# Kernel optimization log

Measured on AMD Instinct MI355X. Metric: run time of the kernel, lower is better.

## Reference

```python
import math
import jax, jax.numpy as jnp
import numpy as np

B, T, C, NH = 2, 2048, 2048, 16
HD = C // NH  # 128


def _quantize_int6(key, out_f, in_f):
    """Replicates Int6LinearDynamic.reset_parameters/_quantize_update."""
    w = jax.random.normal(key, (out_f, in_f), jnp.float32) * (1.0 / math.sqrt(in_f))
    max_val = jnp.clip(jnp.max(jnp.abs(w), axis=1, keepdims=True), 1e-5)
    scale = max_val / 31.0
    w_int = jnp.clip(jnp.round(w / scale), -32, 31).astype(jnp.int8)
    return w_int, scale.squeeze(1)  # [out,in] int8, [out] f32


def setup_inputs() -> dict:
    key = jax.random.key(0)
    k_x, k_a, k_p = jax.random.split(key, 3)
    attn_w, attn_scales = _quantize_int6(k_a, 3 * C, C)
    proj_w, proj_scales = _quantize_int6(k_p, C, C)
    return {
        "x": jax.random.normal(k_x, (B, T, C), jnp.float32),
        "attn_w": attn_w,
        "attn_scales": attn_scales,
        "proj_w": proj_w,
        "proj_scales": proj_scales,
        "qk_gain": jnp.float32(1.0),
    }


def _l2norm(t):
    # F.normalize(p=2, dim=-1, eps=1e-12)
    n = jnp.sqrt(jnp.sum(t * t, axis=-1, keepdims=True))
    return t / jnp.maximum(n, 1e-12)


def reference(x, attn_w, attn_scales, proj_w, proj_scales, qk_gain):
    # dequantized int6 GEMM: w = int8 * per-row scale
    wa = attn_w.astype(jnp.float32) * attn_scales[:, None]  # [3C, C]
    qkv = jnp.einsum("btc,oc->bto", x, wa)                   # [B,T,3C]
    q, k, v = jnp.split(qkv, 3, axis=2)

    def heads(t):  # [B,T,C] -> [B,NH,T,HD]
        return t.reshape(B, T, NH, HD).transpose(0, 2, 1, 3)

    q, k, v = heads(q), heads(k), heads(v)
    q = _l2norm(q) * qk_gain
    k = _l2norm(k) * qk_gain

    # causal SDPA, default scale 1/sqrt(head_dim)
    scores = jnp.einsum("bhqd,bhkd->bhqk", q, k) / math.sqrt(HD)
    causal = jnp.tril(jnp.ones((T, T), dtype=bool))
    scores = jnp.where(causal, scores, -jnp.inf)
    attn = jax.nn.softmax(scores, axis=-1)
    y = jnp.einsum("bhqk,bhkd->bhqd", attn, v)               # [B,NH,T,HD]
    y = y.transpose(0, 2, 1, 3).reshape(B, T, C)

    wp = proj_w.astype(jnp.float32) * proj_scales[:, None]   # [C, C]
    return jnp.einsum("btc,oc->bto", y, wp)
```

## Files before the change

### kernel.cpp

```cpp
#include <hip/hip_runtime.h>


#define DEVINL __device__ __forceinline__

typedef unsigned short u16;
typedef __bf16 bf16x8 __attribute__((ext_vector_type(8)));
typedef float  f32x4  __attribute__((ext_vector_type(4)));
typedef float  f32x16 __attribute__((ext_vector_type(16)));
typedef short  short8 __attribute__((ext_vector_type(8)));
typedef u16    u16x4  __attribute__((ext_vector_type(4)));
typedef unsigned uint4x __attribute__((ext_vector_type(4)));

static constexpr int T_  = 2048;
static constexpr int C_  = 2048;
static constexpr int TC3 = 6144;

DEVINL u16 f2bf(float f) {
  union { float f; unsigned u; } v; v.f = f;
  unsigned r = v.u + 0x7FFFu + ((v.u >> 16) & 1u);
  return (u16)(r >> 16);
}
DEVINL float bf2f(u16 s) {
  union { unsigned u; float f; } v; v.u = ((unsigned)s) << 16;
  return v.f;
}
DEVINL bf16x8 ld8(const u16* p) {
  return __builtin_bit_cast(bf16x8, *(const short8*)p);
}
DEVINL f32x4 mfma16(bf16x8 a, bf16x8 b, f32x4 c) {
  return __builtin_amdgcn_mfma_f32_16x16x32_bf16(a, b, c, 0, 0, 0);
}
DEVINL f32x16 mfma32(bf16x8 a, bf16x8 b, f32x16 c) {
  return __builtin_amdgcn_mfma_f32_32x32x16_bf16(a, b, c, 0, 0, 0);
}
DEVINL void async_cp16(const u16* gp, u16* lp) {
  __builtin_amdgcn_global_load_lds(
      (const __attribute__((address_space(1))) void*)gp,
      (__attribute__((address_space(3))) void*)lp, 16, 0, 0);
}
DEVINL unsigned cvtpk(float lo, float hi) {
  unsigned r;
  asm("v_cvt_pk_bf16_f32 %0, %1, %2" : "=v"(r) : "v"(lo), "v"(hi));
  return r;
}
DEVINL void plswap(unsigned& a, unsigned& b) {
  asm("v_permlane32_swap_b32 %0, %1" : "+v"(a), "+v"(b));
}
template<int N> DEVINL void vmwait() {
  if constexpr (N == 0)      asm volatile("s_waitcnt vmcnt(0)" ::: "memory");
  else if constexpr (N == 5) asm volatile("s_waitcnt vmcnt(5)" ::: "memory");
  else if constexpr (N == 7) asm volatile("s_waitcnt vmcnt(7)" ::: "memory");
  else if constexpr (N == 9) asm volatile("s_waitcnt vmcnt(9)" ::: "memory");
}

__global__ __launch_bounds__(256) void k_cast_x(const float* __restrict__ in,
                                                u16* __restrict__ out) {
  long i = (long)(blockIdx.x * 256 + threadIdx.x) * 4;
  float4 v = *(const float4*)(in + i);
  u16x4 o; o.x = f2bf(v.x); o.y = f2bf(v.y); o.z = f2bf(v.z); o.w = f2bf(v.w);
  *(u16x4*)(out + i) = o;
}
__global__ __launch_bounds__(256) void k_cast_w(const int* __restrict__ in,
                                                u16* __restrict__ out) {
  long i = (long)(blockIdx.x * 256 + threadIdx.x) * 4;
  int4 v = *(const int4*)(in + i);
  u16x4 o; o.x = f2bf((float)v.x); o.y = f2bf((float)v.y);
  o.z = f2bf((float)v.z); o.w = f2bf((float)v.w);
  *(u16x4*)(out + i) = o;
}

template<bool OUT_BF16>
__global__ __launch_bounds__(256) void k_gemm_bt(
    const u16* __restrict__ A, const u16* __restrict__ Bt,
    const float* __restrict__ scale, void* __restrict__ Cv,
    int N, long K) {
  __shared__ u16 As[128 * 32];
  __shared__ u16 Bs[128 * 32];
  const int tid  = threadIdx.x;
  const int wave = tid >> 6;
  const int lane = tid & 63;
  const int l15  = lane & 15;
  const int quad = lane >> 4;
  const int wm = (wave & 1) * 64;
  const int wn = (wave >> 1) * 64;
  const long bm = (long)blockIdx.y * 128;
  const long bn = (long)blockIdx.x * 128;

  f32x4 acc[4][4] = {};

  const int srow = lane >> 2;
  const int scol = (lane & 3) * 8;

  for (long k0 = 0; k0 < K; k0 += 32) {
#pragma unroll
    for (int i = 0; i < 2; ++i) {
      const int j = wave * 2 + i;
      const int row = j * 16 + srow;
      async_cp16(A  + (bm + row) * K + k0 + scol, &As[j * 512]);
      async_cp16(Bt + (bn + row) * K + k0 + scol, &Bs[j * 512]);
    }
    __syncthreads();
    bf16x8 af[4], bfr[4];
#pragma unroll
    for (int mi = 0; mi < 4; ++mi)
      af[mi] = ld8(&As[(wm + mi * 16 + l15) * 32 + quad * 8]);
#pragma unroll
    for (int ni = 0; ni < 4; ++ni)
      bfr[ni] = ld8(&Bs[(wn + ni * 16 + l15) * 32 + quad * 8]);
#pragma unroll
    for (int mi = 0; mi < 4; ++mi)
#pragma unroll
      for (int ni = 0; ni < 4; ++ni)
        acc[mi][ni] = mfma16(af[mi], bfr[ni], acc[mi][ni]);
    __syncthreads();
  }
#pragma unroll
  for (int ni = 0; ni < 4; ++ni) {
    const long col = bn + wn + ni * 16 + l15;
    const float sc = scale[col];
#pragma unroll
    for (int mi = 0; mi < 4; ++mi) {
      const long row0 = bm + wm + mi * 16 + quad * 4;
#pragma unroll
      for (int r = 0; r < 4; ++r) {
        float v = acc[mi][ni][r] * sc;
        if constexpr (OUT_BF16) ((u16*)Cv)[(row0 + r) * (long)N + col] = f2bf(v);
        else                    ((float*)Cv)[(row0 + r) * (long)N + col] = v;
      }
    }
  }
}

template<int SZ>
DEVINL void stage_q(const u16* __restrict__ G, long brow, long K, int tt, int qi,
                    u16 (&L)[2][SZ], int w, int lane) {
  const int sr = w * 8 + (lane >> 3);
  const int sc = lane & 7;
  const long grow = brow + qi * 64 + sr;
  async_cp16(G + grow * K + (long)(tt << 6) + ((sc ^ (sr & 7)) << 3),
             &L[tt & 1][(qi * 64 + w * 8) * 64]);
}

template<int WP1, int WP3, bool ISS0, bool ISS123, bool LAST>
DEVINL void kstep256(int t, const u16* __restrict__ A, const u16* __restrict__ Bt,
                     long K, long bm, long bn,
                     u16 (&As)[2][256 * 64], u16 (&Bs)[2][192 * 64],
                     f32x4 (&acc)[8][3], int w, int lane) {
  const int l15 = lane & 15, quad = lane >> 4;
  const int wm = (w & 1) * 128;
  const int wn = (w >> 1) * 48;
  const int buf = t & 1;

  auto rdA = [&](int mi, int kc) -> bf16x8 {
    const int row = wm + mi * 16 + l15;
    const int k0 = kc * 32 + quad * 8;
    return ld8(&As[buf][row * 64 + (k0 ^ ((row & 7) * 8))]);
  };
  auto rdB = [&](int ni, int kc) -> bf16x8 {
    const int row = wn + ni * 16 + l15;
    const int k0 = kc * 32 + quad * 8;
    return ld8(&Bs[buf][row * 64 + (k0 ^ ((row & 7) * 8))]);
  };

  bf16x8 af[4][2], bfl[2][2];
#pragma unroll
  for (int mi = 0; mi < 4; ++mi) { af[mi][0] = rdA(mi, 0); af[mi][1] = rdA(mi, 1); }
#pragma unroll
  for (int ni = 0; ni < 2; ++ni) { bfl[ni][0] = rdB(ni, 0); bfl[ni][1] = rdB(ni, 1); }
  if constexpr (ISS0) {
    stage_q(A, bm, K, t + 1, 1, As, w, lane);
    stage_q(A, bm, K, t + 1, 3, As, w, lane);
  }
  __builtin_amdgcn_s_barrier();
  __builtin_amdgcn_s_setprio(1);
#pragma unroll
  for (int mi = 0; mi < 4; ++mi)
#pragma unroll
    for (int ni = 0; ni < 2; ++ni) {
      acc[mi][ni] = mfma16(af[mi][0], bfl[ni][0], acc[mi][ni]);
      acc[mi][ni] = mfma16(af[mi][1], bfl[ni][1], acc[mi][ni]);
    }
  __builtin_amdgcn_s_setprio(0);
  __builtin_amdgcn_s_barrier();

  bf16x8 bfh[2];
  bfh[0] = rdB(2, 0); bfh[1] = rdB(2, 1);
  if constexpr (ISS123) {
    stage_q(A, bm, K, t + 2, 0, As, w, lane);
    stage_q(A, bm, K, t + 2, 2, As, w, lane);
  }
  __builtin_amdgcn_s_barrier();
  __builtin_amdgcn_s_setprio(1);
#pragma unroll
  for (int mi = 0; mi < 4; ++mi) {
    acc[mi][2] = mfma16(af[mi][0], bfh[0], acc[mi][2]);
    acc[mi][2] = mfma16(af[mi][1], bfh[1], acc[mi][2]);
  }
  __builtin_amdgcn_s_setprio(0);
  vmwait<WP1>();
  __builtin_amdgcn_s_barrier();

  bf16x8 af2[4][2];
#pragma unroll
  for (int mi = 0; mi < 4; ++mi) { af2[mi][0] = rdA(4 + mi, 0); af2[mi][1] = rdA(4 + mi, 1); }
  if constexpr (ISS123) {
    stage_q(Bt, bn, K, t + 2, 0, Bs, w, lane);
    stage_q(Bt, bn, K, t + 2, 1, Bs, w, lane);
  }
  __builtin_amdgcn_s_barrier();
  __builtin_amdgcn_s_setprio(1);
#pragma unroll
  for (int mi = 0; mi < 4; ++mi) {
    acc[4 + mi][2] = mfma16(af2[mi][0], bfh[0], acc[4 + mi][2]);
    acc[4 + mi][2] = mfma16(af2[mi][1], bfh[1], acc[4 + mi][2]);
  }
  __builtin_amdgcn_s_setprio(0);
  __builtin_amdgcn_s_barrier();

  if constexpr (ISS123) {
    stage_q(Bt, bn, K, t + 2, 2, Bs, w, lane);
  }
  __builtin_amdgcn_s_setprio(1);
#pragma unroll
  for (int mi = 0; mi < 4; ++mi)
#pragma unroll
    for (int ni = 0; ni < 2; ++ni) {
      acc[4 + mi][ni] = mfma16(af2[mi][0], bfl[ni][0], acc[4 + mi][ni]);
      acc[4 + mi][ni] = mfma16(af2[mi][1], bfl[ni][1], acc[4 + mi][ni]);
    }
  __builtin_amdgcn_s_setprio(0);
  if constexpr (!LAST) {
    vmwait<WP3>();
    __builtin_amdgcn_s_barrier();
  }
}

__global__ __launch_bounds__(512, 2) void k_gemm256(
    const u16* __restrict__ A, const u16* __restrict__ Bt,
    const float* __restrict__ scale, u16* __restrict__ C,
    int N, long K) {
  __shared__ u16 As[2][256 * 64];
  __shared__ u16 Bs[2][192 * 64];
  const int tid = threadIdx.x, w = tid >> 6, lane = tid & 63;
  const long bm = (long)blockIdx.y * 256;
  const long bn = (long)blockIdx.x * 192;
  const int nt = (int)(K >> 6);

  stage_q(A, bm, K, 0, 0, As, w, lane); stage_q(A, bm, K, 0, 2, As, w, lane);
  stage_q(Bt, bn, K, 0, 0, Bs, w, lane); stage_q(Bt, bn, K, 0, 1, Bs, w, lane);
  stage_q(Bt, bn, K, 0, 2, Bs, w, lane);
  stage_q(A, bm, K, 0, 1, As, w, lane); stage_q(A, bm, K, 0, 3, As, w, lane);
  stage_q(A, bm, K, 1, 0, As, w, lane); stage_q(A, bm, K, 1, 2, As, w, lane);
  stage_q(Bt, bn, K, 1, 0, Bs, w, lane); stage_q(Bt, bn, K, 1, 1, Bs, w, lane);
  stage_q(Bt, bn, K, 1, 2, Bs, w, lane);
  vmwait<5>();
  __builtin_amdgcn_s_barrier();

  f32x4 acc[8][3] = {};
  int t = 0;
  for (; t < nt - 2; ++t)
    kstep256<9, 5, true, true, false>(t, A, Bt, K, bm, bn, As, Bs, acc, w, lane);
  kstep256<7, 0, true, false, false>(nt - 2, A, Bt, K, bm, bn, As, Bs, acc, w, lane);
  kstep256<0, 0, false, false, true>(nt - 1, A, Bt, K, bm, bn, As, Bs, acc, w, lane);

  const int l15 = lane & 15, quad = lane >> 4;
  const int wm = (w & 1) * 128, wn = (w >> 1) * 48;
#pragma unroll
  for (int ni = 0; ni < 3; ++ni) {
    const long col = bn + wn + ni * 16 + l15;
    const float sc = scale[col];
#pragma unroll
    for (int mi = 0; mi < 8; ++mi) {
      const long row0 = bm + wm + mi * 16 + quad * 4;
#pragma unroll
      for (int r = 0; r < 4; ++r)
        C[(row0 + r) * (long)N + col] = f2bf(acc[mi][ni][r] * sc);
    }
  }
}

__global__ __launch_bounds__(256) void k_norm_qk(u16* __restrict__ qkv,
                                                 const float* __restrict__ qk_gain) {
  const int token = blockIdx.x;
  const int wave = threadIdx.x >> 6, lane = threadIdx.x & 63;
  const float g = qk_gain[0];
  const float qmul = g * g * 1.44269504f * 0.08838834764f;
  u16* rowp = qkv + (long)token * TC3;
#pragma unroll
  for (int s = 0; s < 8; ++s) {
    const int seg = wave * 8 + s;
    const int isK = seg >> 4;
    const int h = seg & 15;
    u16* ptr = rowp + isK * C_ + h * 128 + lane * 2;
    unsigned pv = *(const unsigned*)ptr;
    float a = bf2f((u16)(pv & 0xffffu));
    float bb = bf2f((u16)(pv >> 16));
    float ss = a * a + bb * bb;
#pragma unroll
    for (int m = 1; m <= 32; m <<= 1) ss += __shfl_xor(ss, m);
    float denom = fmaxf(sqrtf(ss), 1e-12f);
    float f = (isK ? 1.0f : qmul) / denom;
    u16 o0 = f2bf(a * f), o1 = f2bf(bb * f);
    *(unsigned*)ptr = (unsigned)o0 | ((unsigned)o1 << 16);
  }
}

__global__ __launch_bounds__(256) void k_vt(const u16* __restrict__ qkv,
                                            u16* __restrict__ vt) {
  const int t0 = blockIdx.x * 64;
  const int h = blockIdx.y, bz = blockIdx.z;
  const int t = threadIdx.x & 63;
  const int d0 = threadIdx.x >> 6;
  const long tokbase = (long)bz * T_;
  const u16* src = qkv + (tokbase + t0 + t) * (long)TC3 + 2 * C_ + h * 128;
  u16* dst = vt + ((long)(bz * 16 + h) * 128) * (long)T_ + t0 + t;
#pragma unroll
  for (int dd = 0; dd < 32; ++dd) {
    const int d = dd * 4 + d0;
    dst[(long)d * T_] = src[d];
  }
}

__global__ __launch_bounds__(256, 2) void k_attn(const u16* __restrict__ qkv,
                                                 const u16* __restrict__ vtg,
                                                 u16* __restrict__ y) {
  const int qt = blockIdx.z ? (15 - blockIdx.x) : blockIdx.x;
  const int h  = blockIdx.y;
  const int bz = blockIdx.z;
  const int tid = threadIdx.x, w = tid >> 6, lane = tid & 63;
  const int m31 = lane & 31, hi = lane >> 5;

  __shared__ u16 Ks[2][64 * 128];
  __shared__ u16 Vt[2][128 * 64];

  const long tokbase = (long)bz * T_;
  const int qbase = qt * 128 + w * 32;
  const u16* vbase = vtg + ((long)(bz * 16 + h) * 128) * (long)T_;
  const u16* kbase = qkv + tokbase * TC3 + C_ + h * 128;

  bf16x8 qf[8];
  {
    const u16* qp = qkv + (tokbase + qbase + m31) * (long)TC3 + h * 128 + hi * 8;
#pragma unroll
    for (int kc = 0; kc < 8; ++kc)
      qf[kc] = ld8(qp + kc * 16);
  }

  f32x16 o[4];
#pragma unroll
  for (int i = 0; i < 4; ++i)
#pragma unroll
    for (int r = 0; r < 16; ++r) o[i][r] = 0.f;
  f32x4 lacc = {0.f, 0.f, 0.f, 0.f};

  auto stage = [&](int ktb, int b) {
#pragma unroll
    for (int j = 0; j < 4; ++j) {
      const int t = w * 4 + j;
      const int p = t * 64 + lane;
      const int r  = p >> 4, ck = p & 15;
      async_cp16(kbase + (long)(ktb + r) * TC3 + ((ck ^ (r & 15)) * 8),
                 &Ks[b][t * 512]);
      const int d  = p >> 3, cv = p & 7;
      async_cp16(vbase + (long)d * T_ + ktb + ((cv ^ (d & 7)) * 8),
                 &Vt[b][t * 512]);
    }
  };

  stage(0, 0);
  __syncthreads();
  int b = 0;
  const int ktmax = 2 * qt + 1;

  for (int kt = 0; kt <= ktmax; ++kt) {
    const int ktb = kt * 64;
    if (kt < ktmax) stage(ktb + 64, b ^ 1);

    if (ktb <= qbase + 31) {
      f32x16 sA[2];
      __builtin_amdgcn_s_setprio(1);
#pragma unroll
      for (int kb = 0; kb < 2; ++kb) {
        f32x16 acc;
#pragma unroll
        for (int r = 0; r < 16; ++r) acc[r] = 0.f;
#pragma unroll
        for (int kc = 0; kc < 8; ++kc) {
          bf16x8 kf = ld8(&Ks[b][(kb * 32 + m31) * 128 +
                                 (((2 * kc + hi) ^ (lane & 15)) * 8)]);
          acc = mfma32(kf, qf[kc], acc);
        }
        sA[kb] = acc;
      }
      __builtin_amdgcn_s_setprio(0);

      if (ktb + 63 > qbase) {
        const int qq = qbase + m31;
#pragma unroll
        for (int kb = 0; kb < 2; ++kb)
#pragma unroll
          for (int r = 0; r < 16; ++r) {
            const int key = ktb + kb * 32 + (r & 3) + 8 * (r >> 2) + 4 * hi;
            if (key > qq) sA[kb][r] = -1e30f;
          }
      }
#pragma unroll
      for (int kb = 0; kb < 2; ++kb)
#pragma unroll
        for (int r = 0; r < 16; ++r) {
          float p = __builtin_amdgcn_exp2f(sA[kb][r]);
          sA[kb][r] = p;
          lacc[r & 3] += p;
        }

      bf16x8 pb[4];
#pragma unroll
      for (int ks = 0; ks < 4; ++ks) {
        const int kb = ks >> 1, j = ks & 1;
        unsigned w0a = cvtpk(sA[kb][8 * j + 0], sA[kb][8 * j + 1]);
        unsigned w1a = cvtpk(sA[kb][8 * j + 2], sA[kb][8 * j + 3]);
        unsigned w0b = cvtpk(sA[kb][8 * j + 4], sA[kb][8 * j + 5]);
        unsigned w1b = cvtpk(sA[kb][8 * j + 6], sA[kb][8 * j + 7]);
        plswap(w0a, w0b);
        plswap(w1a, w1b);
        uint4x t; t.x = w0a; t.y = w1a; t.z = w0b; t.w = w1b;
        pb[ks] = __builtin_bit_cast(bf16x8, t);
      }

      __builtin_amdgcn_s_setprio(1);
#pragma unroll
      for (int db = 0; db < 4; ++db)
#pragma unroll
        for (int ks = 0; ks < 4; ++ks) {
          bf16x8 vf = ld8(&Vt[b][(db * 32 + m31) * 64 +
                                 (((2 * ks + hi) ^ (m31 & 7)) * 8)]);
          o[db] = mfma32(vf, pb[ks], o[db]);
        }
      __builtin_amdgcn_s_setprio(0);
    }

    if (kt < ktmax) __syncthreads();
    b ^= 1;
  }

  float lrow = lacc[0] + lacc[1] + lacc[2] + lacc[3];
  lrow += __shfl_xor(lrow, 32);
  const float inv_l = 1.0f / lrow;
  u16* yp = y + (tokbase + qbase + m31) * (long)C_ + h * 128 + 4 * hi;
#pragma unroll
  for (int db = 0; db < 4; ++db)
#pragma unroll
    for (int g = 0; g < 4; ++g) {
      u16x4 pk;
#pragma unroll
      for (int r = 0; r < 4; ++r) pk[r] = f2bf(o[db][g * 4 + r] * inv_l);
      *(u16x4*)(yp + db * 32 + g * 8) = pk;
    }
}

extern "C" void kernel_launch(void* const* d_in, const int* in_sizes, int n_in,
                              void* d_out, int out_size, void* d_ws, size_t ws_size,
                              hipStream_t stream) {
  const float* x    = (const float*)d_in[0];
  const int*   aw   = (const int*)d_in[1];
  const float* asc  = (const float*)d_in[2];
  const int*   pw   = (const int*)d_in[3];
  const float* psc  = (const float*)d_in[4];
  const float* gain = (const float*)d_in[5];

  char* ws = (char*)d_ws;
  u16* xb  = (u16*)(ws);
  u16* wab = (u16*)(ws + 16777216UL);
  u16* wpb = (u16*)(ws + 41943040UL);
  u16* qkv = (u16*)(ws + 50331648UL);
  u16* yb  = (u16*)(ws + 100663296UL);
  u16* vtg = xb;

  k_cast_x<<<8192, 256, 0, stream>>>(x, xb);
  k_cast_w<<<12288, 256, 0, stream>>>(aw, wab);
  k_cast_w<<<4096, 256, 0, stream>>>(pw, wpb);
  k_gemm256<<<dim3(32, 16), 512, 0, stream>>>(xb, wab, asc, qkv, TC3, (long)C_);
  k_norm_qk<<<4096, 256, 0, stream>>>(qkv, gain);
  k_vt<<<dim3(32, 16, 2), 256, 0, stream>>>(qkv, vtg);
  k_attn<<<dim3(16, 16, 2), 256, 0, stream>>>(qkv, vtg, yb);
  k_gemm_bt<false><<<dim3(16, 32), 256, 0, stream>>>(yb, wpb, psc, (float*)d_out, C_, (long)C_);
}
```

Measured before the change: 419.4 us.

## Re-tile GEMM warps to 64x96 and restructure the K-step staging schedule

Changes the per-wave tile of the 256x192 GEMM from 128x48 to 64x96, using a 4x2 wave grid, and splits each 64-wide K step into two 32-wide halves with four MFMA phases. B-tile staging for step t+1 moves into the current step while A's next-next quarters are issued later, and the prologue and wait counts change to match. The aim is better LDS fragment reuse per MFMA, since each wave now reads fewer bytes per unit of work, and a more even spread of loads between the barriers. The risk is that the shorter prefetch distance for B exposes load latency, and the extra barriers add synchronisation overhead.

```diff
diff --git a/kernel.cpp b/kernel.cpp
--- a/kernel.cpp
+++ b/kernel.cpp
@@ -48,9 +48,7 @@
 }
 template<int N> DEVINL void vmwait() {
   if constexpr (N == 0)      asm volatile("s_waitcnt vmcnt(0)" ::: "memory");
-  else if constexpr (N == 5) asm volatile("s_waitcnt vmcnt(5)" ::: "memory");
-  else if constexpr (N == 7) asm volatile("s_waitcnt vmcnt(7)" ::: "memory");
-  else if constexpr (N == 9) asm volatile("s_waitcnt vmcnt(9)" ::: "memory");
+  else if constexpr (N == 2) asm volatile("s_waitcnt vmcnt(2)" ::: "memory");
 }
 
 __global__ __launch_bounds__(256) void k_cast_x(const float* __restrict__ in,
@@ -141,14 +139,14 @@
              &L[tt & 1][(qi * 64 + w * 8) * 64]);
 }
 
-template<int WP1, int WP3, bool ISS0, bool ISS123, bool LAST>
+template<int WEND, bool ISS1, bool ISS2, bool LAST>
 DEVINL void kstep256(int t, const u16* __restrict__ A, const u16* __restrict__ Bt,
                      long K, long bm, long bn,
                      u16 (&As)[2][256 * 64], u16 (&Bs)[2][192 * 64],
-                     f32x4 (&acc)[8][3], int w, int lane) {
+                     f32x4 (&acc)[4][6], int w, int lane) {
   const int l15 = lane & 15, quad = lane >> 4;
-  const int wm = (w & 1) * 128;
-  const int wn = (w >> 1) * 48;
+  const int wm = (w & 3) * 64;
+  const int wn = (w >> 2) * 96;
   const int buf = t & 1;
 
   auto rdA = [&](int mi, int kc) -> bf16x8 {
@@ -162,75 +160,75 @@
     return ld8(&Bs[buf][row * 64 + (k0 ^ ((row & 7) * 8))]);
   };
 
-  bf16x8 af[4][2], bfl[2][2];
-#pragma unroll
-  for (int mi = 0; mi < 4; ++mi) { af[mi][0] = rdA(mi, 0); af[mi][1] = rdA(mi, 1); }
-#pragma unroll
-  for (int ni = 0; ni < 2; ++ni) { bfl[ni][0] = rdB(ni, 0); bfl[ni][1] = rdB(ni, 1); }
-  if constexpr (ISS0) {
+  bf16x8 aK0[4], aK1[4], bK0[6], bK1[6];
+
+  if constexpr (ISS1) {
     stage_q(A, bm, K, t + 1, 1, As, w, lane);
     stage_q(A, bm, K, t + 1, 3, As, w, lane);
   }
+#pragma unroll
+  for (int mi = 0; mi < 4; ++mi) aK0[mi] = rdA(mi, 0);
+#pragma unroll
+  for (int ni = 0; ni < 3; ++ni) bK0[ni] = rdB(ni, 0);
   __builtin_amdgcn_s_barrier();
   __builtin_amdgcn_s_setprio(1);
 #pragma unroll
   for (int mi = 0; mi < 4; ++mi)
 #pragma unroll
-    for (int ni = 0; ni < 2; ++ni) {
-      acc[mi][ni] = mfma16(af[mi][0], bfl[ni][0], acc[mi][ni]);
-      acc[mi][ni] = mfma16(af[mi][1], bfl[ni][1], acc[mi][ni]);
-    }
+    for (int ni = 0; ni < 3; ++ni)
+      acc[mi][ni] = mfma16(aK0[mi], bK0[ni], acc[mi][ni]);
   __builtin_amdgcn_s_setprio(0);
   __builtin_amdgcn_s_barrier();
 
-  bf16x8 bfh[2];
-  bfh[0] = rdB(2, 0); bfh[1] = rdB(2, 1);
-  if constexpr (ISS123) {
+  if constexpr (ISS1) {
+    stage_q(Bt, bn, K, t + 1, 0, Bs, w, lane);
+    stage_q(Bt, bn, K, t + 1, 1, Bs, w, lane);
+  }
+#pragma unroll
+  for (int ni = 3; ni < 6; ++ni) bK0[ni] = rdB(ni, 0);
+#pragma unroll
+  for (int mi = 0; mi < 4; ++mi) aK1[mi] = rdA(mi, 1);
+  __builtin_amdgcn_s_barrier();
+  __builtin_amdgcn_s_setprio(1);
+#pragma unroll
+  for (int mi = 0; mi < 4; ++mi)
+#pragma unroll
+    for (int ni = 3; ni < 6; ++ni)
+      acc[mi][ni] = mfma16(aK0[mi], bK0[ni], acc[mi][ni]);
+  __builtin_amdgcn_s_setprio(0);
+  __builtin_amdgcn_s_barrier();
+
+  if constexpr (ISS1) {
+    stage_q(Bt, bn, K, t + 1, 2, Bs, w, lane);
+  }
+#pragma unroll
+  for (int ni = 0; ni < 3; ++ni) bK1[ni] = rdB(ni, 1);
+  __builtin_amdgcn_s_barrier();
+  __builtin_amdgcn_s_setprio(1);
+#pragma unroll
+  for (int mi = 0; mi < 4; ++mi)
+#pragma unroll
+    for (int ni = 0; ni < 3; ++ni)
+      acc[mi][ni] = mfma16(aK1[mi], bK1[ni], acc[mi][ni]);
+  __builtin_amdgcn_s_setprio(0);
+  __builtin_amdgcn_s_barrier();
+
+  if constexpr (ISS2) {
     stage_q(A, bm, K, t + 2, 0, As, w, lane);
     stage_q(A, bm, K, t + 2, 2, As, w, lane);
   }
+#pragma unroll
+  for (int ni = 3; ni < 6; ++ni) bK1[ni] = rdB(ni, 1);
   __builtin_amdgcn_s_barrier();
   __builtin_amdgcn_s_setprio(1);
 #pragma unroll
-  for (int mi = 0; mi < 4; ++mi) {
-    acc[mi][2] = mfma16(af[mi][0], bfh[0], acc[mi][2]);
-    acc[mi][2] = mfma16(af[mi][1], bfh[1], acc[mi][2]);
-  }
-  __builtin_amdgcn_s_setprio(0);
-  vmwait<WP1>();
-  __builtin_amdgcn_s_barrier();
-
-  bf16x8 af2[4][2];
-#pragma unroll
-  for (int mi = 0; mi < 4; ++mi) { af2[mi][0] = rdA(4 + mi, 0); af2[mi][1] = rdA(4 + mi, 1); }
-  if constexpr (ISS123) {
-    stage_q(Bt, bn, K, t + 2, 0, Bs, w, lane);
-    stage_q(Bt, bn, K, t + 2, 1, Bs, w, lane);
-  }
-  __builtin_amdgcn_s_barrier();
-  __builtin_amdgcn_s_setprio(1);
-#pragma unroll
-  for (int mi = 0; mi < 4; ++mi) {
-    acc[4 + mi][2] = mfma16(af2[mi][0], bfh[0], acc[4 + mi][2]);
-    acc[4 + mi][2] = mfma16(af2[mi][1], bfh[1], acc[4 + mi][2]);
-  }
-  __builtin_amdgcn_s_setprio(0);
-  __builtin_amdgcn_s_barrier();
-
-  if constexpr (ISS123) {
-    stage_q(Bt, bn, K, t + 2, 2, Bs, w, lane);
-  }
-  __builtin_amdgcn_s_setprio(1);
-#pragma unroll
   for (int mi = 0; mi < 4; ++mi)
 #pragma unroll
-    for (int ni = 0; ni < 2; ++ni) {
-      acc[4 + mi][ni] = mfma16(af2[mi][0], bfl[ni][0], acc[4 + mi][ni]);
-      acc[4 + mi][ni] = mfma16(af2[mi][1], bfl[ni][1], acc[4 + mi][ni]);
-    }
+    for (int ni = 3; ni < 6; ++ni)
+      acc[mi][ni] = mfma16(aK1[mi], bK1[ni], acc[mi][ni]);
   __builtin_amdgcn_s_setprio(0);
   if constexpr (!LAST) {
-    vmwait<WP3>();
+    vmwait<WEND>();
     __builtin_amdgcn_s_barrier();
   }
 }
@@ -247,30 +245,28 @@
   const int nt = (int)(K >> 6);
 
   stage_q(A, bm, K, 0, 0, As, w, lane); stage_q(A, bm, K, 0, 2, As, w, lane);
+  stage_q(A, bm, K, 0, 1, As, w, lane); stage_q(A, bm, K, 0, 3, As, w, lane);
   stage_q(Bt, bn, K, 0, 0, Bs, w, lane); stage_q(Bt, bn, K, 0, 1, Bs, w, lane);
   stage_q(Bt, bn, K, 0, 2, Bs, w, lane);
-  stage_q(A, bm, K, 0, 1, As, w, lane); stage_q(A, bm, K, 0, 3, As, w, lane);
   stage_q(A, bm, K, 1, 0, As, w, lane); stage_q(A, bm, K, 1, 2, As, w, lane);
-  stage_q(Bt, bn, K, 1, 0, Bs, w, lane); stage_q(Bt, bn, K, 1, 1, Bs, w, lane);
-  stage_q(Bt, bn, K, 1, 2, Bs, w, lane);
-  vmwait<5>();
-  __builtin_amdgcn_s_barrier();
-
-  f32x4 acc[8][3] = {};
+  vmwait<2>();
+  __builtin_amdgcn_s_barrier();
+
+  f32x4 acc[4][6] = {};
   int t = 0;
   for (; t < nt - 2; ++t)
-    kstep256<9, 5, true, true, false>(t, A, Bt, K, bm, bn, As, Bs, acc, w, lane);
-  kstep256<7, 0, true, false, false>(nt - 2, A, Bt, K, bm, bn, As, Bs, acc, w, lane);
-  kstep256<0, 0, false, false, true>(nt - 1, A, Bt, K, bm, bn, As, Bs, acc, w, lane);
+    kstep256<2, true, true, false>(t, A, Bt, K, bm, bn, As, Bs, acc, w, lane);
+  kstep256<0, true, false, false>(nt - 2, A, Bt, K, bm, bn, As, Bs, acc, w, lane);
+  kstep256<0, false, false, true>(nt - 1, A, Bt, K, bm, bn, As, Bs, acc, w, lane);
 
   const int l15 = lane & 15, quad = lane >> 4;
-  const int wm = (w & 1) * 128, wn = (w >> 1) * 48;
-#pragma unroll
-  for (int ni = 0; ni < 3; ++ni) {
+  const int wm = (w & 3) * 64, wn = (w >> 2) * 96;
+#pragma unroll
+  for (int ni = 0; ni < 6; ++ni) {
     const long col = bn + wn + ni * 16 + l15;
     const float sc = scale[col];
 #pragma unroll
-    for (int mi = 0; mi < 8; ++mi) {
+    for (int mi = 0; mi < 4; ++mi) {
       const long row0 = bm + wm + mi * 16 + quad * 4;
 #pragma unroll
       for (int r = 0; r < 4; ++r)
```

Result: slower. 451.0 us (+7.6%).
